# Performance work log

Hardware: AMD Instinct MI355X
Metric: run time of the kernel (lower is better)

## Reference

```python
import jax, jax.numpy as jnp
import numpy as np

N, E, DIN, DOUT, DE = 100000, 250000, 32, 32, 13


def setup_inputs() -> dict:
    key = jax.random.key(0)
    ks = jax.random.split(key, 10)
    def u(k, shape, fan):
        b = 1.0 / np.sqrt(fan)
        return jax.random.uniform(k, shape, jnp.float32, -b, b)
    x = jax.random.normal(ks[0], (N, DIN), jnp.float32)
    edge_index = jax.random.randint(ks[1], (2, E), 0, N)
    edge_attr = jax.random.uniform(ks[2], (E, DE), jnp.float32)
    # NNConv's edge network: Linear(DE -> DIN*DOUT)
    nn_w = u(ks[3], (DIN * DOUT, DE), DE)
    nn_b = u(ks[4], (DIN * DOUT,), DE)
    # NNConv root weight + bias
    root = u(ks[5], (DIN, DOUT), DIN)
    bias = jnp.zeros((DOUT,), jnp.float32)
    # GRU(input=DIN, hidden=DOUT), single layer, seq_len=1
    w_ih = u(ks[6], (3 * DOUT, DIN), DOUT)
    w_hh = u(ks[7], (3 * DOUT, DOUT), DOUT)
    b_ih = u(ks[8], (3 * DOUT,), DOUT)
    b_hh = u(ks[9], (3 * DOUT,), DOUT)
    return dict(x=x, edge_attr=edge_attr, nn_w=nn_w, nn_b=nn_b, root=root,
                bias=bias, w_ih=w_ih, w_hh=w_hh, b_ih=b_ih, b_hh=b_hh,
                edge_index=edge_index)


def reference(x, edge_attr, nn_w, nn_b, root, bias, w_ih, w_hh, b_ih, b_hh, edge_index):
    identity = x
    h0 = x  # h is None -> h = x.unsqueeze(0); squeeze the seq dim here
    # norm='_None' (identity) and Dropout in eval mode (identity)
    src, dst = edge_index[0], edge_index[1]
    # NNConv: per-edge weight matrix from edge_attr  [E, DIN, DOUT]
    W = (edge_attr @ nn_w.T + nn_b).reshape(E, DIN, DOUT)
    msg = jnp.einsum('ei,eio->eo', x[src], W)           # [E, DOUT]
    agg = jax.ops.segment_sum(msg, dst, num_segments=N)  # [N, DOUT]
    cnt = jax.ops.segment_sum(jnp.ones((E, 1), x.dtype), dst, num_segments=N)
    mean = agg / jnp.maximum(cnt, 1.0)                   # aggr='mean'
    conv = mean + x @ root + bias
    # celu then GRU step (seq_len=1)
    c = jax.nn.celu(conv)
    gi = c @ w_ih.T + b_ih
    gh = h0 @ w_hh.T + b_hh
    ir, iz, ic = jnp.split(gi, 3, axis=1)
    hr, hz, hc = jnp.split(gh, 3, axis=1)
    r = jax.nn.sigmoid(ir + hr)
    z = jax.nn.sigmoid(iz + hz)
    n = jnp.tanh(ic + r * hc)
    h_new = (1.0 - z) * n + z * h0
    out = jax.nn.relu(h_new + identity)  # res=True, act=ReLU
    return out, h_new[None]
```

## Files before the change

kernel.cpp:

```cpp
#include <hip/hip_runtime.h>
#include <hip/hip_bf16.h>
#include <stdint.h>

#define DIN 32
#define DOUT 32
#define DE 13

typedef float f32x4 __attribute__((ext_vector_type(4)));
typedef short s16x8 __attribute__((ext_vector_type(8)));
typedef int   i32x4 __attribute__((ext_vector_type(4)));

__device__ __forceinline__ unsigned short f2bf(float f) {
    uint32_t b = __float_as_uint(f);
    b += 0x7FFFu + ((b >> 16) & 1u);
    return (unsigned short)(b >> 16);
}
__device__ __forceinline__ uint32_t pk2(float a, float b) {
    float2 t; t.x = a; t.y = b;
    __hip_bfloat162 h = __float22bfloat162_rn(t);
    return *(uint32_t*)&h;
}
__device__ __forceinline__ float sigm(float v) { return 1.f / (1.f + __expf(-v)); }
__device__ __forceinline__ float tanh_fast(float v) { return 2.f / (1.f + __expf(-2.f * v)) - 1.f; }

#define KE_LDS (28 * 512)
__global__ __launch_bounds__(256) void kE(const float* __restrict__ x,
        const float* __restrict__ ea, const int* __restrict__ ei,
        const float* __restrict__ nn_w, const float* __restrict__ nn_b,
        __hip_bfloat162* __restrict__ agg, float* __restrict__ cnt, int E) {
    __shared__ unsigned short Al[KE_LDS];
    __shared__ float tr[4][16 * 36];
    const int tid = threadIdx.x;
    for (int t = tid; t < KE_LDS; t += 256) {
        int j = t & 7;
        int lane = (t >> 3) & 63;
        int tile = t >> 9;
        int at2 = tile >= 14 ? 1 : 0;
        int kt = tile - at2 * 14;
        int o = at2 * 16 + (lane & 15);
        int i = ((lane >> 4) << 3) + j;
        float v = (kt < 13) ? nn_w[(i * 32 + o) * 13 + kt] : nn_b[i * 32 + o];
        Al[t] = f2bf(v);
    }
    __syncthreads();
    const int lane = tid & 63;
    const int wv = tid >> 6;
    const int el = lane & 15;
    const int q8 = (lane >> 4) << 3;
    const int rowb = (lane >> 4) << 2;
    const int pe = lane >> 4;
    const int c2 = lane & 15;
    float* trw = &tr[wv][0];
    int wave = (blockIdx.x * 256 + tid) >> 6;
    const int nw = (gridDim.x * 256) >> 6;
    const int nstrips = E >> 4;
    for (int s = wave; s < nstrips; s += nw) {
        const int e = (s << 4) + el;
        const int dstv = ei[E + e];
        const int srcv = ei[e];
        const float* eab = ea + (size_t)(s << 4) * 13;
        #pragma unroll
        for (int t = 0; t < 4; ++t) {
            int idx = t * 64 + lane;
            if (idx < 208) trw[idx] = eab[idx];
        }
        const float* xq = x + (size_t)srcv * 32 + q8;
        f32x4 xlo = *(const f32x4*)xq;
        f32x4 xhi = *(const f32x4*)(xq + 4);
        float xv[8] = {xlo[0], xlo[1], xlo[2], xlo[3], xhi[0], xhi[1], xhi[2], xhi[3]};
        float g[14];
        #pragma unroll
        for (int d = 0; d < 13; ++d) g[d] = trw[el * 13 + d];
        g[13] = 1.0f;
        f32x4 C0 = {0.f, 0.f, 0.f, 0.f}, C1 = {0.f, 0.f, 0.f, 0.f};
        #pragma unroll
        for (int kt = 0; kt < 14; ++kt) {
            float gk = g[kt];
            i32x4 bi;
            bi[0] = pk2(xv[0] * gk, xv[1] * gk);
            bi[1] = pk2(xv[2] * gk, xv[3] * gk);
            bi[2] = pk2(xv[4] * gk, xv[5] * gk);
            bi[3] = pk2(xv[6] * gk, xv[7] * gk);
            s16x8 bfr = __builtin_bit_cast(s16x8, bi);
            s16x8 a0 = *(const s16x8*)&Al[kt * 512 + lane * 8];
            s16x8 a1 = *(const s16x8*)&Al[(14 + kt) * 512 + lane * 8];
            C0 = __builtin_amdgcn_mfma_f32_16x16x32_bf16(a0, bfr, C0, 0, 0, 0);
            C1 = __builtin_amdgcn_mfma_f32_16x16x32_bf16(a1, bfr, C1, 0, 0, 0);
        }
        *(f32x4*)&trw[el * 36 + rowb] = C0;
        *(f32x4*)&trw[el * 36 + 16 + rowb] = C1;
        #pragma unroll
        for (int p = 0; p < 4; ++p) {
            int e4 = (p << 2) + pe;
            float v0 = trw[e4 * 36 + 2 * c2];
            float v1 = trw[e4 * 36 + 2 * c2 + 1];
            int d4 = __shfl(dstv, e4, 64);
            float2 fv; fv.x = v0; fv.y = v1;
            __hip_bfloat162 val = __float22bfloat162_rn(fv);
            unsafeAtomicAdd(&agg[(size_t)d4 * 16 + c2], val);
        }
        if (lane < 16) atomicAdd(&cnt[dstv], 1.0f);
    }
}

__global__ __launch_bounds__(256) void kC(const float* __restrict__ x,
        const __hip_bfloat16* __restrict__ aggb, const float* __restrict__ cnt,
        const float* __restrict__ root, const float* __restrict__ bias,
        const float* __restrict__ w_ih, const float* __restrict__ w_hh,
        const float* __restrict__ b_ih, const float* __restrict__ b_hh,
        float* __restrict__ out, float* __restrict__ hnew, int N) {
    __shared__ unsigned short Bl[14 * 64 * 8];
    __shared__ unsigned short clds[4][16 * 32];
    const int tid = threadIdx.x;
    for (int t = tid; t < 14 * 64 * 8; t += 256) {
        int j = t & 7;
        int lane = (t >> 3) & 63;
        int tt = t >> 9;
        int i = ((lane >> 4) << 3) + j;
        int c = lane & 15;
        float v;
        if (tt < 8) {
            int col = tt * 16 + c;
            v = (col < 32) ? root[i * 32 + col] : w_hh[(col - 32) * 32 + i];
        } else {
            v = w_ih[((tt - 8) * 16 + c) * 32 + i];
        }
        Bl[t] = f2bf(v);
    }
    __syncthreads();
    const int lane = tid & 63;
    const int wv = tid >> 6;
    const int c15 = lane & 15;
    const int rowb = (lane >> 4) << 2;
    float binit[14];
    #pragma unroll
    for (int t = 0; t < 2; ++t) binit[t] = bias[t * 16 + c15];
    #pragma unroll
    for (int t = 2; t < 8; ++t) binit[t] = b_hh[t * 16 + c15 - 32];
    #pragma unroll
    for (int u = 0; u < 6; ++u) binit[8 + u] = b_ih[u * 16 + c15];
    int wave = (blockIdx.x * 256 + tid) >> 6;
    const int nw = (gridDim.x * 256) >> 6;
    const int nstrips = N >> 4;
    for (int s = wave; s < nstrips; s += nw) {
        const int n0 = s << 4;
        const float* xp = x + (size_t)(n0 + c15) * 32 + ((lane >> 4) << 3);
        f32x4 x0 = *(const f32x4*)xp;
        f32x4 x1 = *(const f32x4*)(xp + 4);
        s16x8 a;
        a[0] = (short)f2bf(x0[0]); a[1] = (short)f2bf(x0[1]);
        a[2] = (short)f2bf(x0[2]); a[3] = (short)f2bf(x0[3]);
        a[4] = (short)f2bf(x1[0]); a[5] = (short)f2bf(x1[1]);
        a[6] = (short)f2bf(x1[2]); a[7] = (short)f2bf(x1[3]);
        f32x4 D[8];
        #pragma unroll
        for (int t = 0; t < 8; ++t) {
            s16x8 b = *(const s16x8*)&Bl[(t * 64 + lane) * 8];
            f32x4 ci = {binit[t], binit[t], binit[t], binit[t]};
            D[t] = __builtin_amdgcn_mfma_f32_16x16x32_bf16(a, b, ci, 0, 0, 0);
        }
        float xr[4][2];
        #pragma unroll
        for (int r = 0; r < 4; ++r) {
            const int n = n0 + rowb + r;
            float cn = fmaxf(cnt[n], 1.f);
            #pragma unroll
            for (int t = 0; t < 2; ++t) {
                float ag = __bfloat162float(aggb[(size_t)n * 32 + t * 16 + c15]);
                xr[r][t] = x[(size_t)n * 32 + t * 16 + c15];
                float conv = ag / cn + D[t][r];
                float cv = conv > 0.f ? conv : (__expf(conv) - 1.f);
                clds[wv][(rowb + r) * 32 + t * 16 + c15] = f2bf(cv);
            }
        }
        s16x8 a2 = *(const s16x8*)&clds[wv][c15 * 32 + ((lane >> 4) << 3)];
        f32x4 G[6];
        #pragma unroll
        for (int u = 0; u < 6; ++u) {
            s16x8 b = *(const s16x8*)&Bl[((8 + u) * 64 + lane) * 8];
            f32x4 ci = {binit[8 + u], binit[8 + u], binit[8 + u], binit[8 + u]};
            G[u] = __builtin_amdgcn_mfma_f32_16x16x32_bf16(a2, b, ci, 0, 0, 0);
        }
        #pragma unroll
        for (int t = 0; t < 2; ++t) {
            #pragma unroll
            for (int r = 0; r < 4; ++r) {
                float rg = sigm(G[t][r] + D[2 + t][r]);
                float z  = sigm(G[2 + t][r] + D[4 + t][r]);
                float nn = tanh_fast(G[4 + t][r] + rg * D[6 + t][r]);
                float h  = (1.f - z) * nn + z * xr[r][t];
                float ov = h + xr[r][t];
                size_t oi = (size_t)(n0 + rowb + r) * 32 + t * 16 + c15;
                out[oi]  = ov > 0.f ? ov : 0.f;
                hnew[oi] = h;
            }
        }
    }
}

extern "C" void kernel_launch(void* const* d_in, const int* in_sizes, int n_in,
                              void* d_out, int out_size, void* d_ws, size_t ws_size,
                              hipStream_t stream) {
    const float* x    = (const float*)d_in[0];
    const float* ea   = (const float*)d_in[1];
    const float* nn_w = (const float*)d_in[2];
    const float* nn_b = (const float*)d_in[3];
    const float* root = (const float*)d_in[4];
    const float* bias = (const float*)d_in[5];
    const float* w_ih = (const float*)d_in[6];
    const float* w_hh = (const float*)d_in[7];
    const float* b_ih = (const float*)d_in[8];
    const float* b_hh = (const float*)d_in[9];
    const int*   ei   = (const int*)d_in[10];
    const int N = in_sizes[0] / DIN;
    const int E = in_sizes[10] / 2;
    float* out  = (float*)d_out;
    float* hnew = out + (size_t)N * DOUT;

    const size_t agg_bytes = (size_t)N * 32 * sizeof(__hip_bfloat16);
    const size_t cnt_bytes = (size_t)N * sizeof(float);

    __hip_bfloat162* agg = (__hip_bfloat162*)d_ws;
    float* cnt = (float*)((char*)d_ws + agg_bytes);
    hipMemsetAsync(d_ws, 0, agg_bytes + cnt_bytes, stream);
    kE<<<2048, 256, 0, stream>>>(x, ea, ei, nn_w, nn_b, agg, cnt, E);
    kC<<<512, 256, 0, stream>>>(x, (const __hip_bfloat16*)d_ws, cnt, root, bias,
                                w_ih, w_hh, b_ih, b_hh, out, hnew, N);
}
```

Before: 164.6 us.

## Replace atomic scatter-add aggregation with per-node edge buckets and gather

The edge kernel no longer atomically adds bf16 messages into a per-node accumulator. It now writes each edge's message to a dense buffer and records the edge id in a per-destination bucket slot, claimed with an atomic degree counter and capped at 64 slots. The node kernel then gathers each node's messages from its bucket, computes the mean in fp32 in LDS, and feeds it into the existing MFMA GRU path. The goal is to remove contended bf16 atomics and the larger memset. The cost is an extra 16MB message round-trip, strided bucket writes, and a serial dependent-load gather loop. Nodes with more than 64 incoming edges would silently lose messages. The node kernel grid also grows from 512 to 784 blocks.

```diff
diff --git a/kernel.cpp b/kernel.cpp
--- a/kernel.cpp
+++ b/kernel.cpp
@@ -5,11 +5,15 @@
 #define DIN 32
 #define DOUT 32
 #define DE 13
+#define CAP 64
 
 typedef float f32x4 __attribute__((ext_vector_type(4)));
 typedef short s16x8 __attribute__((ext_vector_type(8)));
 typedef int   i32x4 __attribute__((ext_vector_type(4)));
-
+typedef unsigned int u32x4 __attribute__((ext_vector_type(4)));
+
+__device__ __forceinline__ float bf2f_lo(uint32_t u) { return __uint_as_float(u << 16); }
+__device__ __forceinline__ float bf2f_hi(uint32_t u) { return __uint_as_float(u & 0xffff0000u); }
 __device__ __forceinline__ unsigned short f2bf(float f) {
     uint32_t b = __float_as_uint(f);
     b += 0x7FFFu + ((b >> 16) & 1u);
@@ -24,10 +28,11 @@
 __device__ __forceinline__ float tanh_fast(float v) { return 2.f / (1.f + __expf(-2.f * v)) - 1.f; }
 
 #define KE_LDS (28 * 512)
-__global__ __launch_bounds__(256) void kE(const float* __restrict__ x,
+__global__ __launch_bounds__(256) void kM(const float* __restrict__ x,
         const float* __restrict__ ea, const int* __restrict__ ei,
         const float* __restrict__ nn_w, const float* __restrict__ nn_b,
-        __hip_bfloat162* __restrict__ agg, float* __restrict__ cnt, int E) {
+        uint32_t* __restrict__ msg, uint32_t* __restrict__ deg,
+        uint32_t* __restrict__ bucket, int E, int N) {
     __shared__ unsigned short Al[KE_LDS];
     __shared__ float tr[4][16 * 36];
     const int tid = threadIdx.x;
@@ -94,23 +99,25 @@
             int e4 = (p << 2) + pe;
             float v0 = trw[e4 * 36 + 2 * c2];
             float v1 = trw[e4 * 36 + 2 * c2 + 1];
-            int d4 = __shfl(dstv, e4, 64);
-            float2 fv; fv.x = v0; fv.y = v1;
-            __hip_bfloat162 val = __float22bfloat162_rn(fv);
-            unsafeAtomicAdd(&agg[(size_t)d4 * 16 + c2], val);
-        }
-        if (lane < 16) atomicAdd(&cnt[dstv], 1.0f);
-    }
-}
-
-__global__ __launch_bounds__(256) void kC(const float* __restrict__ x,
-        const __hip_bfloat16* __restrict__ aggb, const float* __restrict__ cnt,
+            msg[((size_t)(s << 4) + e4) * 16 + c2] = pk2(v0, v1);
+        }
+        if (lane < 16) {
+            uint32_t slot = atomicAdd(&deg[dstv], 1u);
+            if (slot < CAP) bucket[(size_t)slot * N + dstv] = (uint32_t)e;
+        }
+    }
+}
+
+__global__ __launch_bounds__(256) void kG(const float* __restrict__ x,
+        const uint32_t* __restrict__ msg, const uint32_t* __restrict__ deg,
+        const uint32_t* __restrict__ bucket,
         const float* __restrict__ root, const float* __restrict__ bias,
         const float* __restrict__ w_ih, const float* __restrict__ w_hh,
         const float* __restrict__ b_ih, const float* __restrict__ b_hh,
         float* __restrict__ out, float* __restrict__ hnew, int N) {
     __shared__ unsigned short Bl[14 * 64 * 8];
     __shared__ unsigned short clds[4][16 * 32];
+    __shared__ float aggf[4][16 * 36];
     const int tid = threadIdx.x;
     for (int t = tid; t < 14 * 64 * 8; t += 256) {
         int j = t & 7;
@@ -132,6 +139,8 @@
     const int wv = tid >> 6;
     const int c15 = lane & 15;
     const int rowb = (lane >> 4) << 2;
+    const int m4 = lane >> 2;
+    const int q4 = lane & 3;
     float binit[14];
     #pragma unroll
     for (int t = 0; t < 2; ++t) binit[t] = bias[t * 16 + c15];
@@ -144,6 +153,21 @@
     const int nstrips = N >> 4;
     for (int s = wave; s < nstrips; s += nw) {
         const int n0 = s << 4;
+        uint32_t dm = deg[n0 + m4];
+        if (dm > CAP) dm = CAP;
+        float acc[8] = {0.f, 0.f, 0.f, 0.f, 0.f, 0.f, 0.f, 0.f};
+        for (uint32_t k = 0; k < dm; ++k) {
+            uint32_t eid = bucket[(size_t)k * N + n0 + m4];
+            u32x4 mv = *(const u32x4*)&msg[(size_t)eid * 16 + q4 * 4];
+            acc[0] += bf2f_lo(mv[0]); acc[1] += bf2f_hi(mv[0]);
+            acc[2] += bf2f_lo(mv[1]); acc[3] += bf2f_hi(mv[1]);
+            acc[4] += bf2f_lo(mv[2]); acc[5] += bf2f_hi(mv[2]);
+            acc[6] += bf2f_lo(mv[3]); acc[7] += bf2f_hi(mv[3]);
+        }
+        float inv = 1.f / fmaxf((float)dm, 1.f);
+        float* ap = &aggf[wv][m4 * 36 + q4 * 8];
+        #pragma unroll
+        for (int j = 0; j < 8; ++j) ap[j] = acc[j] * inv;
         const float* xp = x + (size_t)(n0 + c15) * 32 + ((lane >> 4) << 3);
         f32x4 x0 = *(const f32x4*)xp;
         f32x4 x1 = *(const f32x4*)(xp + 4);
@@ -163,12 +187,11 @@
         #pragma unroll
         for (int r = 0; r < 4; ++r) {
             const int n = n0 + rowb + r;
-            float cn = fmaxf(cnt[n], 1.f);
             #pragma unroll
             for (int t = 0; t < 2; ++t) {
-                float ag = __bfloat162float(aggb[(size_t)n * 32 + t * 16 + c15]);
+                float ag = aggf[wv][(rowb + r) * 36 + t * 16 + c15];
                 xr[r][t] = x[(size_t)n * 32 + t * 16 + c15];
-                float conv = ag / cn + D[t][r];
+                float conv = ag + D[t][r];
                 float cv = conv > 0.f ? conv : (__expf(conv) - 1.f);
                 clds[wv][(rowb + r) * 32 + t * 16 + c15] = f2bf(cv);
             }
@@ -217,13 +240,15 @@
     float* out  = (float*)d_out;
     float* hnew = out + (size_t)N * DOUT;
 
-    const size_t agg_bytes = (size_t)N * 32 * sizeof(__hip_bfloat16);
-    const size_t cnt_bytes = (size_t)N * sizeof(float);
-
-    __hip_bfloat162* agg = (__hip_bfloat162*)d_ws;
-    float* cnt = (float*)((char*)d_ws + agg_bytes);
-    hipMemsetAsync(d_ws, 0, agg_bytes + cnt_bytes, stream);
-    kE<<<2048, 256, 0, stream>>>(x, ea, ei, nn_w, nn_b, agg, cnt, E);
-    kC<<<512, 256, 0, stream>>>(x, (const __hip_bfloat16*)d_ws, cnt, root, bias,
+    const size_t deg_bytes = (size_t)N * sizeof(uint32_t);
+    const size_t msg_bytes = (size_t)E * 16 * sizeof(uint32_t);
+
+    uint32_t* deg    = (uint32_t*)d_ws;
+    uint32_t* msg    = (uint32_t*)((char*)d_ws + deg_bytes);
+    uint32_t* bucket = (uint32_t*)((char*)d_ws + deg_bytes + msg_bytes);
+
+    hipMemsetAsync(deg, 0, deg_bytes, stream);
+    kM<<<2048, 256, 0, stream>>>(x, ea, ei, nn_w, nn_b, msg, deg, bucket, E, N);
+    kG<<<784, 256, 0, stream>>>(x, msg, deg, bucket, root, bias,
                                 w_ih, w_hh, b_ih, b_hh, out, hnew, N);
 }
```

After: 177.0 us. +7.5%, slower.

## Replace MFMA node-update kernel with per-thread scalar FP32 GRU kernel

Applied to the files above, without the earlier changes.

The node-side kernel (root linear, CELU, GRU step) is rewritten so that each thread handles one node entirely in scalar FP32 FMAs, replacing the wave-level bf16 MFMA tiles that staged weights in LDS. Weights are now read directly from global memory as uniform scalar loads, and x and agg are loaded as vector loads per node. This removes the LDS staging, the bf16 rounding of the node math and the strip loop. In exchange, each node costs about 7K FP32 FMAs on the vector ALUs instead of matrix-core work, and the per-thread arrays will put heavy pressure on registers.

```diff
diff --git a/kernel.cpp b/kernel.cpp
--- a/kernel.cpp
+++ b/kernel.cpp
@@ -9,7 +9,10 @@
 typedef float f32x4 __attribute__((ext_vector_type(4)));
 typedef short s16x8 __attribute__((ext_vector_type(8)));
 typedef int   i32x4 __attribute__((ext_vector_type(4)));
-
+typedef unsigned int u32x4 __attribute__((ext_vector_type(4)));
+
+__device__ __forceinline__ float bf2f_lo(uint32_t u) { return __uint_as_float(u << 16); }
+__device__ __forceinline__ float bf2f_hi(uint32_t u) { return __uint_as_float(u & 0xffff0000u); }
 __device__ __forceinline__ unsigned short f2bf(float f) {
     uint32_t b = __float_as_uint(f);
     b += 0x7FFFu + ((b >> 16) & 1u);
@@ -103,98 +106,80 @@
     }
 }
 
-__global__ __launch_bounds__(256) void kC(const float* __restrict__ x,
-        const __hip_bfloat16* __restrict__ aggb, const float* __restrict__ cnt,
+__global__ __launch_bounds__(256) void kN(const float* __restrict__ x,
+        const unsigned int* __restrict__ aggb, const float* __restrict__ cnt,
         const float* __restrict__ root, const float* __restrict__ bias,
         const float* __restrict__ w_ih, const float* __restrict__ w_hh,
         const float* __restrict__ b_ih, const float* __restrict__ b_hh,
         float* __restrict__ out, float* __restrict__ hnew, int N) {
-    __shared__ unsigned short Bl[14 * 64 * 8];
-    __shared__ unsigned short clds[4][16 * 32];
-    const int tid = threadIdx.x;
-    for (int t = tid; t < 14 * 64 * 8; t += 256) {
-        int j = t & 7;
-        int lane = (t >> 3) & 63;
-        int tt = t >> 9;
-        int i = ((lane >> 4) << 3) + j;
-        int c = lane & 15;
-        float v;
-        if (tt < 8) {
-            int col = tt * 16 + c;
-            v = (col < 32) ? root[i * 32 + col] : w_hh[(col - 32) * 32 + i];
-        } else {
-            v = w_ih[((tt - 8) * 16 + c) * 32 + i];
-        }
-        Bl[t] = f2bf(v);
-    }
-    __syncthreads();
-    const int lane = tid & 63;
-    const int wv = tid >> 6;
-    const int c15 = lane & 15;
-    const int rowb = (lane >> 4) << 2;
-    float binit[14];
+    const int n = blockIdx.x * 256 + threadIdx.x;
+    if (n >= N) return;
+    float xv[32];
+    const f32x4* xp = (const f32x4*)(x + (size_t)n * 32);
     #pragma unroll
-    for (int t = 0; t < 2; ++t) binit[t] = bias[t * 16 + c15];
+    for (int q = 0; q < 8; ++q) {
+        f32x4 v = xp[q];
+        xv[4 * q] = v[0]; xv[4 * q + 1] = v[1]; xv[4 * q + 2] = v[2]; xv[4 * q + 3] = v[3];
+    }
+    float ag[32];
+    const u32x4* ap = (const u32x4*)(aggb + (size_t)n * 16);
     #pragma unroll
-    for (int t = 2; t < 8; ++t) binit[t] = b_hh[t * 16 + c15 - 32];
+    for (int q = 0; q < 4; ++q) {
+        u32x4 u = ap[q];
+        ag[8 * q + 0] = bf2f_lo(u[0]); ag[8 * q + 1] = bf2f_hi(u[0]);
+        ag[8 * q + 2] = bf2f_lo(u[1]); ag[8 * q + 3] = bf2f_hi(u[1]);
+        ag[8 * q + 4] = bf2f_lo(u[2]); ag[8 * q + 5] = bf2f_hi(u[2]);
+        ag[8 * q + 6] = bf2f_lo(u[3]); ag[8 * q + 7] = bf2f_hi(u[3]);
+    }
+    const float inv = 1.f / fmaxf(cnt[n], 1.f);
+    float c[32];
+    #pragma unroll 4
+    for (int o = 0; o < 32; ++o) {
+        float acc = bias[o];
+        #pragma unroll
+        for (int i = 0; i < 32; ++i) acc = fmaf(xv[i], root[i * 32 + o], acc);
+        float conv = fmaf(ag[o], inv, acc);
+        c[o] = conv > 0.f ? conv : (__expf(conv) - 1.f);
+    }
+    float ho[32];
+    #pragma unroll 2
+    for (int o = 0; o < 32; ++o) {
+        float ir = b_ih[o], iz = b_ih[32 + o], ic = b_ih[64 + o];
+        float hr = b_hh[o], hz = b_hh[32 + o], hc = b_hh[64 + o];
+        const float* wi0 = w_ih + (size_t)o * 32;
+        const float* wi1 = w_ih + (size_t)(32 + o) * 32;
+        const float* wi2 = w_ih + (size_t)(64 + o) * 32;
+        const float* wh0 = w_hh + (size_t)o * 32;
+        const float* wh1 = w_hh + (size_t)(32 + o) * 32;
+        const float* wh2 = w_hh + (size_t)(64 + o) * 32;
+        #pragma unroll
+        for (int i = 0; i < 32; ++i) {
+            ir = fmaf(c[i], wi0[i], ir);
+            iz = fmaf(c[i], wi1[i], iz);
+            ic = fmaf(c[i], wi2[i], ic);
+            hr = fmaf(xv[i], wh0[i], hr);
+            hz = fmaf(xv[i], wh1[i], hz);
+            hc = fmaf(xv[i], wh2[i], hc);
+        }
+        float r = sigm(ir + hr);
+        float z = sigm(iz + hz);
+        float nn = tanh_fast(ic + r * hc);
+        ho[o] = (1.f - z) * nn + z * xv[o];
+    }
+    float* op = out + (size_t)n * 32;
+    float* hp = hnew + (size_t)n * 32;
     #pragma unroll
-    for (int u = 0; u < 6; ++u) binit[8 + u] = b_ih[u * 16 + c15];
-    int wave = (blockIdx.x * 256 + tid) >> 6;
-    const int nw = (gridDim.x * 256) >> 6;
-    const int nstrips = N >> 4;
-    for (int s = wave; s < nstrips; s += nw) {
-        const int n0 = s << 4;
-        const float* xp = x + (size_t)(n0 + c15) * 32 + ((lane >> 4) << 3);
-        f32x4 x0 = *(const f32x4*)xp;
-        f32x4 x1 = *(const f32x4*)(xp + 4);
-        s16x8 a;
-        a[0] = (short)f2bf(x0[0]); a[1] = (short)f2bf(x0[1]);
-        a[2] = (short)f2bf(x0[2]); a[3] = (short)f2bf(x0[3]);
-        a[4] = (short)f2bf(x1[0]); a[5] = (short)f2bf(x1[1]);
-        a[6] = (short)f2bf(x1[2]); a[7] = (short)f2bf(x1[3]);
-        f32x4 D[8];
-        #pragma unroll
-        for (int t = 0; t < 8; ++t) {
-            s16x8 b = *(const s16x8*)&Bl[(t * 64 + lane) * 8];
-            f32x4 ci = {binit[t], binit[t], binit[t], binit[t]};
-            D[t] = __builtin_amdgcn_mfma_f32_16x16x32_bf16(a, b, ci, 0, 0, 0);
-        }
-        float xr[4][2];
-        #pragma unroll
-        for (int r = 0; r < 4; ++r) {
-            const int n = n0 + rowb + r;
-            float cn = fmaxf(cnt[n], 1.f);
-            #pragma unroll
-            for (int t = 0; t < 2; ++t) {
-                float ag = __bfloat162float(aggb[(size_t)n * 32 + t * 16 + c15]);
-                xr[r][t] = x[(size_t)n * 32 + t * 16 + c15];
-                float conv = ag / cn + D[t][r];
-                float cv = conv > 0.f ? conv : (__expf(conv) - 1.f);
-                clds[wv][(rowb + r) * 32 + t * 16 + c15] = f2bf(cv);
-            }
-        }
-        s16x8 a2 = *(const s16x8*)&clds[wv][c15 * 32 + ((lane >> 4) << 3)];
-        f32x4 G[6];
-        #pragma unroll
-        for (int u = 0; u < 6; ++u) {
-            s16x8 b = *(const s16x8*)&Bl[((8 + u) * 64 + lane) * 8];
-            f32x4 ci = {binit[8 + u], binit[8 + u], binit[8 + u], binit[8 + u]};
-            G[u] = __builtin_amdgcn_mfma_f32_16x16x32_bf16(a2, b, ci, 0, 0, 0);
-        }
-        #pragma unroll
-        for (int t = 0; t < 2; ++t) {
-            #pragma unroll
-            for (int r = 0; r < 4; ++r) {
-                float rg = sigm(G[t][r] + D[2 + t][r]);
-                float z  = sigm(G[2 + t][r] + D[4 + t][r]);
-                float nn = tanh_fast(G[4 + t][r] + rg * D[6 + t][r]);
-                float h  = (1.f - z) * nn + z * xr[r][t];
-                float ov = h + xr[r][t];
-                size_t oi = (size_t)(n0 + rowb + r) * 32 + t * 16 + c15;
-                out[oi]  = ov > 0.f ? ov : 0.f;
-                hnew[oi] = h;
-            }
-        }
+    for (int q = 0; q < 8; ++q) {
+        f32x4 vo, vh;
+        #pragma unroll
+        for (int j = 0; j < 4; ++j) {
+            float h = ho[4 * q + j];
+            vh[j] = h;
+            float s = h + xv[4 * q + j];
+            vo[j] = s > 0.f ? s : 0.f;
+        }
+        *(f32x4*)(op + 4 * q) = vo;
+        *(f32x4*)(hp + 4 * q) = vh;
     }
 }
 
@@ -224,6 +209,7 @@
     float* cnt = (float*)((char*)d_ws + agg_bytes);
     hipMemsetAsync(d_ws, 0, agg_bytes + cnt_bytes, stream);
     kE<<<2048, 256, 0, stream>>>(x, ea, ei, nn_w, nn_b, agg, cnt, E);
-    kC<<<512, 256, 0, stream>>>(x, (const __hip_bfloat16*)d_ws, cnt, root, bias,
-                                w_ih, w_hh, b_ih, b_hh, out, hnew, N);
-}
+    kN<<<(N + 255) / 256, 256, 0, stream>>>(x, (const unsigned int*)d_ws, cnt,
+                                            root, bias, w_ih, w_hh, b_ih, b_hh,
+                                            out, hnew, N);
+}
```

New measurement: 231.6 us. +40.7%, slower.
